# Performance work log

Measured on AMD Instinct MI355X. Metric: run time of the kernel, lower is better.

## Reference

```python
import jax, jax.numpy as jnp
import numpy as np


def setup_inputs() -> dict:
    key = jax.random.key(0)
    k1, k2, k3, k4, k5 = jax.random.split(key, 5)
    b, t_q, t_k = 4, 256, 1024
    qs, ms, n = 512, 512, 128
    return {
        "query": jax.random.normal(k1, (b, t_q, qs), dtype=jnp.float32),
        "keys": jax.random.normal(k2, (b, t_k, ms), dtype=jnp.float32),
        "Wq": jax.random.normal(k3, (qs, n), dtype=jnp.float32) * 0.05,
        "Wk": jax.random.normal(k4, (ms, n), dtype=jnp.float32) * 0.05,
        "linear_att": jax.random.normal(k5, (n,), dtype=jnp.float32) * 0.05,
    }


def reference(query, keys, Wq, Wk, linear_att):
    # projections: b t_q n and b t_k n
    att_query = jnp.einsum("bqd,dn->bqn", query, Wq)
    att_keys = jnp.einsum("bkd,dn->bkn", keys, Wk)
    # Bahdanau additive score: tanh(q + k) . v  -> b t_q t_k
    sum_qk = att_query[:, :, None, :] + att_keys[:, None, :, :]
    scores = jnp.einsum("bqkn,n->bqk", jnp.tanh(sum_qk), linear_att)
    weights = jax.nn.softmax(scores, axis=-1)
    context = jnp.einsum("bqk,bkd->bqd", weights, keys)
    return (context, weights)
```

## Files before the change

kernel.cpp:

```cpp
#include <hip/hip_runtime.h>

#define B 4
#define TQ 256
#define TK 1024
#define QS 512
#define NN 128

#define TANH_SCALE 2.8853900817779268f
#define LOG2E 1.4426950408889634f

__device__ __forceinline__ float fast_exp2(float x) {
#if __has_builtin(__builtin_amdgcn_exp2f)
    return __builtin_amdgcn_exp2f(x);
#else
    return exp2f(x);
#endif
}
__device__ __forceinline__ float fast_rcp(float x) {
#if __has_builtin(__builtin_amdgcn_rcpf)
    return __builtin_amdgcn_rcpf(x);
#else
    return 1.0f / x;
#endif
}

__global__ __launch_bounds__(256) void proj_kernel(
    const float* __restrict__ query, const float* __restrict__ keys,
    const float* __restrict__ Wq, const float* __restrict__ Wk,
    float* __restrict__ attq, float* __restrict__ attkT)
{
    __shared__ float As[32][18];
    __shared__ float Bs[32][132];

    const int tid = threadIdx.x;
    const int rb = blockIdx.x * 16;
    const bool isq = (rb < B * TQ);
    const float* A = isq ? (query + (size_t)rb * QS)
                         : (keys + (size_t)(rb - B * TQ) * QS);
    const float* W = isq ? Wq : Wk;

    const int n0 = (tid & 31) * 4;
    const int q0 = (tid >> 5) * 2;
    float acc[2][4] = {};

    for (int k0 = 0; k0 < QS; k0 += 32) {
        {
            const int r = tid >> 4, c = tid & 15;
            const float2 v = *(const float2*)(A + (size_t)r * QS + k0 + c * 2);
            As[c * 2 + 0][r] = v.x;
            As[c * 2 + 1][r] = v.y;
        }
        {
            const int n = (tid & 31) * 4, r0 = tid >> 5;
            #pragma unroll
            for (int j = 0; j < 4; ++j) {
                const int kk = r0 + j * 8;
                *(float4*)&Bs[kk][n] =
                    *(const float4*)(W + (size_t)(k0 + kk) * NN + n);
            }
        }
        __syncthreads();
        #pragma unroll
        for (int kk = 0; kk < 32; ++kk) {
            const float2 a = *(const float2*)&As[kk][q0];
            const float4 b = *(const float4*)&Bs[kk][n0];
            acc[0][0] = fmaf(a.x, b.x, acc[0][0]);
            acc[0][1] = fmaf(a.x, b.y, acc[0][1]);
            acc[0][2] = fmaf(a.x, b.z, acc[0][2]);
            acc[0][3] = fmaf(a.x, b.w, acc[0][3]);
            acc[1][0] = fmaf(a.y, b.x, acc[1][0]);
            acc[1][1] = fmaf(a.y, b.y, acc[1][1]);
            acc[1][2] = fmaf(a.y, b.z, acc[1][2]);
            acc[1][3] = fmaf(a.y, b.w, acc[1][3]);
        }
        __syncthreads();
    }

    if (isq) {
        float* out = attq + (size_t)rb * NN;
        #pragma unroll
        for (int i = 0; i < 2; ++i) {
            float4 o;
            o.x = acc[i][0] * TANH_SCALE;
            o.y = acc[i][1] * TANH_SCALE;
            o.z = acc[i][2] * TANH_SCALE;
            o.w = acc[i][3] * TANH_SCALE;
            *(float4*)(out + (size_t)(q0 + i) * NN + n0) = o;
        }
    } else {
        #pragma unroll
        for (int i = 0; i < 2; ++i) {
            float4 o;
            o.x = acc[i][0] * TANH_SCALE;
            o.y = acc[i][1] * TANH_SCALE;
            o.z = acc[i][2] * TANH_SCALE;
            o.w = acc[i][3] * TANH_SCALE;
            *(float4*)&Bs[q0 + i][n0] = o;
        }
        __syncthreads();
        const int rk = rb - B * TQ;
        const int bb = rk >> 10;
        const int kbase = rk & 1023;
        const int n = tid >> 1;
        const int kh = (tid & 1) * 8;
        float* o = attkT + (size_t)bb * NN * TK + (size_t)n * TK + kbase + kh;
        #pragma unroll
        for (int m4 = 0; m4 < 2; ++m4) {
            float4 t;
            t.x = Bs[kh + m4 * 4 + 0][n];
            t.y = Bs[kh + m4 * 4 + 1][n];
            t.z = Bs[kh + m4 * 4 + 2][n];
            t.w = Bs[kh + m4 * 4 + 3][n];
            *(float4*)(o + m4 * 4) = t;
        }
    }
}

__global__ __launch_bounds__(256) void score_softmax_kernel(
    const float* __restrict__ attq, const float* __restrict__ attkT,
    const float* __restrict__ vatt, float* __restrict__ wout)
{
    __shared__ float aqs[2][128];
    __shared__ float vsm[128];
    __shared__ float red[2][8];

    const int tid = threadIdx.x;
    const int b = blockIdx.x >> 7;
    const int q0 = (blockIdx.x & 127) * 2;

    if (tid < 128) {
        aqs[0][tid] = attq[((size_t)b * TQ + q0) * NN + tid];
        vsm[tid] = vatt[tid];
    } else {
        aqs[1][tid & 127] = attq[((size_t)b * TQ + q0 + 1) * NN + (tid & 127)];
    }
    __syncthreads();

    const float* kt = attkT + (size_t)b * NN * TK + (size_t)tid * 4;
    float s[2][4] = {};

    #pragma unroll 8
    for (int n = 0; n < 128; ++n) {
        const float4 a = *(const float4*)(kt + (size_t)n * TK);
        const float a0 = aqs[0][n], a1 = aqs[1][n], vv = vsm[n];
        const float av[4] = {a.x, a.y, a.z, a.w};
        #pragma unroll
        for (int r = 0; r < 4; ++r) {
            const float x0 = a0 + av[r];
            const float t0 = fmaf(-2.f, fast_rcp(1.f + fast_exp2(x0)), 1.f);
            s[0][r] = fmaf(vv, t0, s[0][r]);
            const float x1 = a1 + av[r];
            const float t1 = fmaf(-2.f, fast_rcp(1.f + fast_exp2(x1)), 1.f);
            s[1][r] = fmaf(vv, t1, s[1][r]);
        }
    }

    const int lane = tid & 63, wid = tid >> 6;
    #pragma unroll
    for (int qq = 0; qq < 2; ++qq) {
        float mm = fmaxf(fmaxf(s[qq][0], s[qq][1]), fmaxf(s[qq][2], s[qq][3]));
        #pragma unroll
        for (int off = 32; off > 0; off >>= 1)
            mm = fmaxf(mm, __shfl_xor(mm, off, 64));
        if (lane == 0) red[qq][wid] = mm;
    }
    __syncthreads();
    float m[2];
    m[0] = fmaxf(fmaxf(red[0][0], red[0][1]), fmaxf(red[0][2], red[0][3]));
    m[1] = fmaxf(fmaxf(red[1][0], red[1][1]), fmaxf(red[1][2], red[1][3]));

    float e[2][4];
    #pragma unroll
    for (int qq = 0; qq < 2; ++qq) {
        float ls = 0.f;
        #pragma unroll
        for (int i = 0; i < 4; ++i) {
            e[qq][i] = fast_exp2((s[qq][i] - m[qq]) * LOG2E);
            ls += e[qq][i];
        }
        #pragma unroll
        for (int off = 32; off > 0; off >>= 1)
            ls += __shfl_xor(ls, off, 64);
        if (lane == 0) red[qq][4 + wid] = ls;
    }
    __syncthreads();
    #pragma unroll
    for (int qq = 0; qq < 2; ++qq) {
        const float S = red[qq][4] + red[qq][5] + red[qq][6] + red[qq][7];
        const float inv = fast_rcp(S);
        float4 w4;
        w4.x = e[qq][0] * inv; w4.y = e[qq][1] * inv;
        w4.z = e[qq][2] * inv; w4.w = e[qq][3] * inv;
        *(float4*)(wout + ((size_t)b * TQ + q0 + qq) * TK + (size_t)tid * 4) = w4;
    }
}

#define CTX_ELEMS ((size_t)B * TQ * QS)

__global__ __launch_bounds__(256) void context_kernel(
    const float* __restrict__ keys, const float* __restrict__ w,
    float* __restrict__ ctxp)
{
    __shared__ float Wst[32][34];
    __shared__ float Ks[32][64];

    const int tid = threadIdx.x;
    const int bid = blockIdx.x;
    const int b = bid >> 8;
    const int rem = bid & 255;
    const int qt = rem >> 5;
    const int dt = (rem >> 2) & 7;
    const int ks = rem & 3;

    const float* wb = w + (size_t)b * TQ * TK + (size_t)qt * 32 * TK + ks * 256;
    const float* kb = keys + (size_t)b * TK * QS + (size_t)ks * 256 * QS + dt * 64;

    const int d0 = (tid & 15) * 4;
    const int q0 = (tid >> 4) * 2;
    float acc[2][4] = {};

    for (int k0 = 0; k0 < 256; k0 += 32) {
        {
            const int r = tid >> 3, c = tid & 7;
            const float4 v = *(const float4*)(wb + (size_t)r * TK + k0 + c * 4);
            Wst[c * 4 + 0][r] = v.x;
            Wst[c * 4 + 1][r] = v.y;
            Wst[c * 4 + 2][r] = v.z;
            Wst[c * 4 + 3][r] = v.w;
        }
        {
            const int c = tid & 15, r = tid >> 4;
            *(float4*)&Ks[r][c * 4] =
                *(const float4*)(kb + (size_t)(k0 + r) * QS + c * 4);
            *(float4*)&Ks[r + 16][c * 4] =
                *(const float4*)(kb + (size_t)(k0 + r + 16) * QS + c * 4);
        }
        __syncthreads();
        #pragma unroll
        for (int kk = 0; kk < 32; ++kk) {
            const float2 a = *(const float2*)&Wst[kk][q0];
            const float4 bb = *(const float4*)&Ks[kk][d0];
            acc[0][0] = fmaf(a.x, bb.x, acc[0][0]);
            acc[0][1] = fmaf(a.x, bb.y, acc[0][1]);
            acc[0][2] = fmaf(a.x, bb.z, acc[0][2]);
            acc[0][3] = fmaf(a.x, bb.w, acc[0][3]);
            acc[1][0] = fmaf(a.y, bb.x, acc[1][0]);
            acc[1][1] = fmaf(a.y, bb.y, acc[1][1]);
            acc[1][2] = fmaf(a.y, bb.z, acc[1][2]);
            acc[1][3] = fmaf(a.y, bb.w, acc[1][3]);
        }
        __syncthreads();
    }

    float* op = ctxp + (size_t)ks * CTX_ELEMS
              + ((size_t)b * TQ + qt * 32 + q0) * QS + dt * 64 + d0;
    #pragma unroll
    for (int i = 0; i < 2; ++i) {
        float4 o;
        o.x = acc[i][0]; o.y = acc[i][1]; o.z = acc[i][2]; o.w = acc[i][3];
        *(float4*)(op + (size_t)i * QS) = o;
    }
}

__global__ __launch_bounds__(256) void reduce_kernel(
    const float4* __restrict__ ctxp, float4* __restrict__ ctx)
{
    const size_t idx = (size_t)blockIdx.x * 256 + threadIdx.x;
    const size_t stride = CTX_ELEMS / 4;
    const float4 a = ctxp[idx];
    const float4 b = ctxp[idx + stride];
    const float4 c = ctxp[idx + 2 * stride];
    const float4 d = ctxp[idx + 3 * stride];
    float4 o;
    o.x = (a.x + b.x) + (c.x + d.x);
    o.y = (a.y + b.y) + (c.y + d.y);
    o.z = (a.z + b.z) + (c.z + d.z);
    o.w = (a.w + b.w) + (c.w + d.w);
    ctx[idx] = o;
}

extern "C" void kernel_launch(void* const* d_in, const int* in_sizes, int n_in,
                              void* d_out, int out_size, void* d_ws, size_t ws_size,
                              hipStream_t stream) {
    const float* query = (const float*)d_in[0];
    const float* keys  = (const float*)d_in[1];
    const float* Wq    = (const float*)d_in[2];
    const float* Wk    = (const float*)d_in[3];
    const float* vatt  = (const float*)d_in[4];

    float* ctx = (float*)d_out;
    float* wts = ctx + CTX_ELEMS;

    float* attq  = (float*)d_ws;
    float* attkT = attq + (size_t)B * TQ * NN;
    float* ctxp  = attkT + (size_t)B * NN * TK;

    hipLaunchKernelGGL(proj_kernel, dim3((B * TQ + B * TK) / 16), dim3(256), 0,
                       stream, query, keys, Wq, Wk, attq, attkT);
    hipLaunchKernelGGL(score_softmax_kernel, dim3(B * TQ / 2), dim3(256), 0,
                       stream, attq, attkT, vatt, wts);
    hipLaunchKernelGGL(context_kernel, dim3(1024), dim3(256), 0,
                       stream, keys, wts, ctxp);
    hipLaunchKernelGGL(reduce_kernel, dim3((unsigned)(CTX_ELEMS / 4 / 256)), dim3(256), 0,
                       stream, (const float4*)ctxp, (float4*)ctx);
}
```

Baseline: 149.5 us.

## Fuse four stage kernels into one cooperative kernel with grid syncs

Replaces the four separate launches (projection, score+softmax, context GEMM, split-K reduce) with a single cooperative kernel of 512 blocks that separates the stages with grid.sync and unions their shared memory. The context stage now splits K two ways instead of four, so the reduce reads only two partials. This removes launch gaps between kernels, but it caps parallelism at 512 resident blocks and adds grid-wide barrier cost. Stages that previously used more blocks (the 1024-block context GEMM) now run with fewer, longer blocks.

```diff
diff --git a/kernel.cpp b/kernel.cpp
--- a/kernel.cpp
+++ b/kernel.cpp
@@ -1,4 +1,7 @@
 #include <hip/hip_runtime.h>
+#include <hip/hip_cooperative_groups.h>
+
+namespace cg = cooperative_groups;
 
 #define B 4
 #define TQ 256
@@ -8,6 +11,7 @@
 
 #define TANH_SCALE 2.8853900817779268f
 #define LOG2E 1.4426950408889634f
+#define CTX_ELEMS ((size_t)B * TQ * QS)
 
 __device__ __forceinline__ float fast_exp2(float x) {
 #if __has_builtin(__builtin_amdgcn_exp2f)
@@ -24,259 +28,261 @@
 #endif
 }
 
-__global__ __launch_bounds__(256) void proj_kernel(
+union SmemU {
+    struct { float As[32][18]; float Bs[32][132]; } p1;
+    struct { float aqs[2][128]; float vsm[128]; float red[2][8]; } p2;
+    struct { float Wst[32][34]; float Ks[32][64]; } p3;
+};
+
+__global__ __launch_bounds__(256, 2) void fused_kernel(
     const float* __restrict__ query, const float* __restrict__ keys,
     const float* __restrict__ Wq, const float* __restrict__ Wk,
-    float* __restrict__ attq, float* __restrict__ attkT)
+    const float* __restrict__ vatt,
+    float* __restrict__ attq, float* __restrict__ attkT,
+    float* __restrict__ ctxp, float* __restrict__ ctx,
+    float* __restrict__ wout)
 {
-    __shared__ float As[32][18];
-    __shared__ float Bs[32][132];
-
+    __shared__ SmemU sm;
+    cg::grid_group grid = cg::this_grid();
     const int tid = threadIdx.x;
-    const int rb = blockIdx.x * 16;
-    const bool isq = (rb < B * TQ);
-    const float* A = isq ? (query + (size_t)rb * QS)
-                         : (keys + (size_t)(rb - B * TQ) * QS);
-    const float* W = isq ? Wq : Wk;
-
-    const int n0 = (tid & 31) * 4;
-    const int q0 = (tid >> 5) * 2;
-    float acc[2][4] = {};
-
-    for (int k0 = 0; k0 < QS; k0 += 32) {
-        {
-            const int r = tid >> 4, c = tid & 15;
-            const float2 v = *(const float2*)(A + (size_t)r * QS + k0 + c * 2);
-            As[c * 2 + 0][r] = v.x;
-            As[c * 2 + 1][r] = v.y;
-        }
-        {
-            const int n = (tid & 31) * 4, r0 = tid >> 5;
-            #pragma unroll
-            for (int j = 0; j < 4; ++j) {
-                const int kk = r0 + j * 8;
-                *(float4*)&Bs[kk][n] =
-                    *(const float4*)(W + (size_t)(k0 + kk) * NN + n);
-            }
+    const int bid = blockIdx.x;
+
+    if (bid < 320) {
+        const int rb = bid * 16;
+        const bool isq = (rb < B * TQ);
+        const float* A = isq ? (query + (size_t)rb * QS)
+                             : (keys + (size_t)(rb - B * TQ) * QS);
+        const float* W = isq ? Wq : Wk;
+
+        const int n0 = (tid & 31) * 4;
+        const int q0 = (tid >> 5) * 2;
+        float acc[2][4] = {};
+
+        for (int k0 = 0; k0 < QS; k0 += 32) {
+            {
+                const int r = tid >> 4, c = tid & 15;
+                const float2 v = *(const float2*)(A + (size_t)r * QS + k0 + c * 2);
+                sm.p1.As[c * 2 + 0][r] = v.x;
+                sm.p1.As[c * 2 + 1][r] = v.y;
+            }
+            {
+                const int n = (tid & 31) * 4, r0 = tid >> 5;
+                #pragma unroll
+                for (int j = 0; j < 4; ++j) {
+                    const int kk = r0 + j * 8;
+                    *(float4*)&sm.p1.Bs[kk][n] =
+                        *(const float4*)(W + (size_t)(k0 + kk) * NN + n);
+                }
+            }
+            __syncthreads();
+            #pragma unroll
+            for (int kk = 0; kk < 32; ++kk) {
+                const float2 a = *(const float2*)&sm.p1.As[kk][q0];
+                const float4 b = *(const float4*)&sm.p1.Bs[kk][n0];
+                acc[0][0] = fmaf(a.x, b.x, acc[0][0]);
+                acc[0][1] = fmaf(a.x, b.y, acc[0][1]);
+                acc[0][2] = fmaf(a.x, b.z, acc[0][2]);
+                acc[0][3] = fmaf(a.x, b.w, acc[0][3]);
+                acc[1][0] = fmaf(a.y, b.x, acc[1][0]);
+                acc[1][1] = fmaf(a.y, b.y, acc[1][1]);
+                acc[1][2] = fmaf(a.y, b.z, acc[1][2]);
+                acc[1][3] = fmaf(a.y, b.w, acc[1][3]);
+            }
+            __syncthreads();
+        }
+
+        if (isq) {
+            float* out = attq + (size_t)rb * NN;
+            #pragma unroll
+            for (int i = 0; i < 2; ++i) {
+                float4 o;
+                o.x = acc[i][0] * TANH_SCALE;
+                o.y = acc[i][1] * TANH_SCALE;
+                o.z = acc[i][2] * TANH_SCALE;
+                o.w = acc[i][3] * TANH_SCALE;
+                *(float4*)(out + (size_t)(q0 + i) * NN + n0) = o;
+            }
+        } else {
+            #pragma unroll
+            for (int i = 0; i < 2; ++i) {
+                float4 o;
+                o.x = acc[i][0] * TANH_SCALE;
+                o.y = acc[i][1] * TANH_SCALE;
+                o.z = acc[i][2] * TANH_SCALE;
+                o.w = acc[i][3] * TANH_SCALE;
+                *(float4*)&sm.p1.Bs[q0 + i][n0] = o;
+            }
+            __syncthreads();
+            const int rk = rb - B * TQ;
+            const int bb = rk >> 10;
+            const int kbase = rk & 1023;
+            const int n = tid >> 1;
+            const int kh = (tid & 1) * 8;
+            float* o = attkT + (size_t)bb * NN * TK + (size_t)n * TK + kbase + kh;
+            #pragma unroll
+            for (int m4 = 0; m4 < 2; ++m4) {
+                float4 t;
+                t.x = sm.p1.Bs[kh + m4 * 4 + 0][n];
+                t.y = sm.p1.Bs[kh + m4 * 4 + 1][n];
+                t.z = sm.p1.Bs[kh + m4 * 4 + 2][n];
+                t.w = sm.p1.Bs[kh + m4 * 4 + 3][n];
+                *(float4*)(o + m4 * 4) = t;
+            }
+        }
+    }
+    __threadfence();
+    grid.sync();
+
+    {
+        const int b = bid >> 7;
+        const int q0 = (bid & 127) * 2;
+
+        if (tid < 128) {
+            sm.p2.aqs[0][tid] = attq[((size_t)b * TQ + q0) * NN + tid];
+            sm.p2.vsm[tid] = vatt[tid];
+        } else {
+            sm.p2.aqs[1][tid & 127] =
+                attq[((size_t)b * TQ + q0 + 1) * NN + (tid & 127)];
+        }
+        __syncthreads();
+
+        const float* kt = attkT + (size_t)b * NN * TK + (size_t)tid * 4;
+        float s[2][4] = {};
+
+        #pragma unroll 8
+        for (int n = 0; n < 128; ++n) {
+            const float4 a = *(const float4*)(kt + (size_t)n * TK);
+            const float a0 = sm.p2.aqs[0][n], a1 = sm.p2.aqs[1][n];
+            const float vv = sm.p2.vsm[n];
+            const float av[4] = {a.x, a.y, a.z, a.w};
+            #pragma unroll
+            for (int r = 0; r < 4; ++r) {
+                const float x0 = a0 + av[r];
+                const float t0 = fmaf(-2.f, fast_rcp(1.f + fast_exp2(x0)), 1.f);
+                s[0][r] = fmaf(vv, t0, s[0][r]);
+                const float x1 = a1 + av[r];
+                const float t1 = fmaf(-2.f, fast_rcp(1.f + fast_exp2(x1)), 1.f);
+                s[1][r] = fmaf(vv, t1, s[1][r]);
+            }
+        }
+
+        const int lane = tid & 63, wid = tid >> 6;
+        #pragma unroll
+        for (int qq = 0; qq < 2; ++qq) {
+            float mm = fmaxf(fmaxf(s[qq][0], s[qq][1]), fmaxf(s[qq][2], s[qq][3]));
+            #pragma unroll
+            for (int off = 32; off > 0; off >>= 1)
+                mm = fmaxf(mm, __shfl_xor(mm, off, 64));
+            if (lane == 0) sm.p2.red[qq][wid] = mm;
+        }
+        __syncthreads();
+        float m[2];
+        m[0] = fmaxf(fmaxf(sm.p2.red[0][0], sm.p2.red[0][1]),
+                     fmaxf(sm.p2.red[0][2], sm.p2.red[0][3]));
+        m[1] = fmaxf(fmaxf(sm.p2.red[1][0], sm.p2.red[1][1]),
+                     fmaxf(sm.p2.red[1][2], sm.p2.red[1][3]));
+
+        float e[2][4];
+        #pragma unroll
+        for (int qq = 0; qq < 2; ++qq) {
+            float ls = 0.f;
+            #pragma unroll
+            for (int i = 0; i < 4; ++i) {
+                e[qq][i] = fast_exp2((s[qq][i] - m[qq]) * LOG2E);
+                ls += e[qq][i];
+            }
+            #pragma unroll
+            for (int off = 32; off > 0; off >>= 1)
+                ls += __shfl_xor(ls, off, 64);
+            if (lane == 0) sm.p2.red[qq][4 + wid] = ls;
         }
         __syncthreads();
         #pragma unroll
-        for (int kk = 0; kk < 32; ++kk) {
-            const float2 a = *(const float2*)&As[kk][q0];
-            const float4 b = *(const float4*)&Bs[kk][n0];
-            acc[0][0] = fmaf(a.x, b.x, acc[0][0]);
-            acc[0][1] = fmaf(a.x, b.y, acc[0][1]);
-            acc[0][2] = fmaf(a.x, b.z, acc[0][2]);
-            acc[0][3] = fmaf(a.x, b.w, acc[0][3]);
-            acc[1][0] = fmaf(a.y, b.x, acc[1][0]);
-            acc[1][1] = fmaf(a.y, b.y, acc[1][1]);
-            acc[1][2] = fmaf(a.y, b.z, acc[1][2]);
-            acc[1][3] = fmaf(a.y, b.w, acc[1][3]);
-        }
-        __syncthreads();
+        for (int qq = 0; qq < 2; ++qq) {
+            const float S = sm.p2.red[qq][4] + sm.p2.red[qq][5] +
+                            sm.p2.red[qq][6] + sm.p2.red[qq][7];
+            const float inv = fast_rcp(S);
+            float4 w4;
+            w4.x = e[qq][0] * inv; w4.y = e[qq][1] * inv;
+            w4.z = e[qq][2] * inv; w4.w = e[qq][3] * inv;
+            *(float4*)(wout + ((size_t)b * TQ + q0 + qq) * TK + (size_t)tid * 4) = w4;
+        }
     }
-
-    if (isq) {
-        float* out = attq + (size_t)rb * NN;
+    __threadfence();
+    grid.sync();
+
+    {
+        const int b = bid >> 7;
+        const int rem = bid & 127;
+        const int qt = rem >> 4;
+        const int dt = (rem >> 1) & 7;
+        const int ks = rem & 1;
+
+        const float* wb = wout + (size_t)b * TQ * TK + (size_t)qt * 32 * TK + ks * 512;
+        const float* kb = keys + (size_t)b * TK * QS + (size_t)ks * 512 * QS + dt * 64;
+
+        const int d0 = (tid & 15) * 4;
+        const int q0 = (tid >> 4) * 2;
+        float acc[2][4] = {};
+
+        for (int k0 = 0; k0 < 512; k0 += 32) {
+            {
+                const int r = tid >> 3, c = tid & 7;
+                const float4 v = *(const float4*)(wb + (size_t)r * TK + k0 + c * 4);
+                sm.p3.Wst[c * 4 + 0][r] = v.x;
+                sm.p3.Wst[c * 4 + 1][r] = v.y;
+                sm.p3.Wst[c * 4 + 2][r] = v.z;
+                sm.p3.Wst[c * 4 + 3][r] = v.w;
+            }
+            {
+                const int c = tid & 15, r = tid >> 4;
+                *(float4*)&sm.p3.Ks[r][c * 4] =
+                    *(const float4*)(kb + (size_t)(k0 + r) * QS + c * 4);
+                *(float4*)&sm.p3.Ks[r + 16][c * 4] =
+                    *(const float4*)(kb + (size_t)(k0 + r + 16) * QS + c * 4);
+            }
+            __syncthreads();
+            #pragma unroll
+            for (int kk = 0; kk < 32; ++kk) {
+                const float2 a = *(const float2*)&sm.p3.Wst[kk][q0];
+                const float4 bb = *(const float4*)&sm.p3.Ks[kk][d0];
+                acc[0][0] = fmaf(a.x, bb.x, acc[0][0]);
+                acc[0][1] = fmaf(a.x, bb.y, acc[0][1]);
+                acc[0][2] = fmaf(a.x, bb.z, acc[0][2]);
+                acc[0][3] = fmaf(a.x, bb.w, acc[0][3]);
+                acc[1][0] = fmaf(a.y, bb.x, acc[1][0]);
+                acc[1][1] = fmaf(a.y, bb.y, acc[1][1]);
+                acc[1][2] = fmaf(a.y, bb.z, acc[1][2]);
+                acc[1][3] = fmaf(a.y, bb.w, acc[1][3]);
+            }
+            __syncthreads();
+        }
+
+        float* op = ctxp + (size_t)ks * CTX_ELEMS
+                  + ((size_t)b * TQ + qt * 32 + q0) * QS + dt * 64 + d0;
         #pragma unroll
         for (int i = 0; i < 2; ++i) {
             float4 o;
-            o.x = acc[i][0] * TANH_SCALE;
-            o.y = acc[i][1] * TANH_SCALE;
-            o.z = acc[i][2] * TANH_SCALE;
-            o.w = acc[i][3] * TANH_SCALE;
-            *(float4*)(out + (size_t)(q0 + i) * NN + n0) = o;
-        }
-    } else {
-        #pragma unroll
-        for (int i = 0; i < 2; ++i) {
-            float4 o;
-            o.x = acc[i][0] * TANH_SCALE;
-            o.y = acc[i][1] * TANH_SCALE;
-            o.z = acc[i][2] * TANH_SCALE;
-            o.w = acc[i][3] * TANH_SCALE;
-            *(float4*)&Bs[q0 + i][n0] = o;
-        }
-        __syncthreads();
-        const int rk = rb - B * TQ;
-        const int bb = rk >> 10;
-        const int kbase = rk & 1023;
-        const int n = tid >> 1;
-        const int kh = (tid & 1) * 8;
-        float* o = attkT + (size_t)bb * NN * TK + (size_t)n * TK + kbase + kh;
-        #pragma unroll
-        for (int m4 = 0; m4 < 2; ++m4) {
-            float4 t;
-            t.x = Bs[kh + m4 * 4 + 0][n];
-            t.y = Bs[kh + m4 * 4 + 1][n];
-            t.z = Bs[kh + m4 * 4 + 2][n];
-            t.w = Bs[kh + m4 * 4 + 3][n];
-            *(float4*)(o + m4 * 4) = t;
+            o.x = acc[i][0]; o.y = acc[i][1]; o.z = acc[i][2]; o.w = acc[i][3];
+            *(float4*)(op + (size_t)i * QS) = o;
         }
     }
-}
-
-__global__ __launch_bounds__(256) void score_softmax_kernel(
-    const float* __restrict__ attq, const float* __restrict__ attkT,
-    const float* __restrict__ vatt, float* __restrict__ wout)
-{
-    __shared__ float aqs[2][128];
-    __shared__ float vsm[128];
-    __shared__ float red[2][8];
-
-    const int tid = threadIdx.x;
-    const int b = blockIdx.x >> 7;
-    const int q0 = (blockIdx.x & 127) * 2;
-
-    if (tid < 128) {
-        aqs[0][tid] = attq[((size_t)b * TQ + q0) * NN + tid];
-        vsm[tid] = vatt[tid];
-    } else {
-        aqs[1][tid & 127] = attq[((size_t)b * TQ + q0 + 1) * NN + (tid & 127)];
+    __threadfence();
+    grid.sync();
+
+    {
+        const size_t idx = (size_t)bid * 256 + tid;
+        const size_t stride = CTX_ELEMS / 4;
+        const float4* p = (const float4*)ctxp;
+        const float4 a = p[idx];
+        const float4 b4 = p[idx + stride];
+        float4 o;
+        o.x = a.x + b4.x;
+        o.y = a.y + b4.y;
+        o.z = a.z + b4.z;
+        o.w = a.w + b4.w;
+        ((float4*)ctx)[idx] = o;
     }
-    __syncthreads();
-
-    const float* kt = attkT + (size_t)b * NN * TK + (size_t)tid * 4;
-    float s[2][4] = {};
-
-    #pragma unroll 8
-    for (int n = 0; n < 128; ++n) {
-        const float4 a = *(const float4*)(kt + (size_t)n * TK);
-        const float a0 = aqs[0][n], a1 = aqs[1][n], vv = vsm[n];
-        const float av[4] = {a.x, a.y, a.z, a.w};
-        #pragma unroll
-        for (int r = 0; r < 4; ++r) {
-            const float x0 = a0 + av[r];
-            const float t0 = fmaf(-2.f, fast_rcp(1.f + fast_exp2(x0)), 1.f);
-            s[0][r] = fmaf(vv, t0, s[0][r]);
-            const float x1 = a1 + av[r];
-            const float t1 = fmaf(-2.f, fast_rcp(1.f + fast_exp2(x1)), 1.f);
-            s[1][r] = fmaf(vv, t1, s[1][r]);
-        }
-    }
-
-    const int lane = tid & 63, wid = tid >> 6;
-    #pragma unroll
-    for (int qq = 0; qq < 2; ++qq) {
-        float mm = fmaxf(fmaxf(s[qq][0], s[qq][1]), fmaxf(s[qq][2], s[qq][3]));
-        #pragma unroll
-        for (int off = 32; off > 0; off >>= 1)
-            mm = fmaxf(mm, __shfl_xor(mm, off, 64));
-        if (lane == 0) red[qq][wid] = mm;
-    }
-    __syncthreads();
-    float m[2];
-    m[0] = fmaxf(fmaxf(red[0][0], red[0][1]), fmaxf(red[0][2], red[0][3]));
-    m[1] = fmaxf(fmaxf(red[1][0], red[1][1]), fmaxf(red[1][2], red[1][3]));
-
-    float e[2][4];
-    #pragma unroll
-    for (int qq = 0; qq < 2; ++qq) {
-        float ls = 0.f;
-        #pragma unroll
-        for (int i = 0; i < 4; ++i) {
-            e[qq][i] = fast_exp2((s[qq][i] - m[qq]) * LOG2E);
-            ls += e[qq][i];
-        }
-        #pragma unroll
-        for (int off = 32; off > 0; off >>= 1)
-            ls += __shfl_xor(ls, off, 64);
-        if (lane == 0) red[qq][4 + wid] = ls;
-    }
-    __syncthreads();
-    #pragma unroll
-    for (int qq = 0; qq < 2; ++qq) {
-        const float S = red[qq][4] + red[qq][5] + red[qq][6] + red[qq][7];
-        const float inv = fast_rcp(S);
-        float4 w4;
-        w4.x = e[qq][0] * inv; w4.y = e[qq][1] * inv;
-        w4.z = e[qq][2] * inv; w4.w = e[qq][3] * inv;
-        *(float4*)(wout + ((size_t)b * TQ + q0 + qq) * TK + (size_t)tid * 4) = w4;
-    }
-}
-
-#define CTX_ELEMS ((size_t)B * TQ * QS)
-
-__global__ __launch_bounds__(256) void context_kernel(
-    const float* __restrict__ keys, const float* __restrict__ w,
-    float* __restrict__ ctxp)
-{
-    __shared__ float Wst[32][34];
-    __shared__ float Ks[32][64];
-
-    const int tid = threadIdx.x;
-    const int bid = blockIdx.x;
-    const int b = bid >> 8;
-    const int rem = bid & 255;
-    const int qt = rem >> 5;
-    const int dt = (rem >> 2) & 7;
-    const int ks = rem & 3;
-
-    const float* wb = w + (size_t)b * TQ * TK + (size_t)qt * 32 * TK + ks * 256;
-    const float* kb = keys + (size_t)b * TK * QS + (size_t)ks * 256 * QS + dt * 64;
-
-    const int d0 = (tid & 15) * 4;
-    const int q0 = (tid >> 4) * 2;
-    float acc[2][4] = {};
-
-    for (int k0 = 0; k0 < 256; k0 += 32) {
-        {
-            const int r = tid >> 3, c = tid & 7;
-            const float4 v = *(const float4*)(wb + (size_t)r * TK + k0 + c * 4);
-            Wst[c * 4 + 0][r] = v.x;
-            Wst[c * 4 + 1][r] = v.y;
-            Wst[c * 4 + 2][r] = v.z;
-            Wst[c * 4 + 3][r] = v.w;
-        }
-        {
-            const int c = tid & 15, r = tid >> 4;
-            *(float4*)&Ks[r][c * 4] =
-                *(const float4*)(kb + (size_t)(k0 + r) * QS + c * 4);
-            *(float4*)&Ks[r + 16][c * 4] =
-                *(const float4*)(kb + (size_t)(k0 + r + 16) * QS + c * 4);
-        }
-        __syncthreads();
-        #pragma unroll
-        for (int kk = 0; kk < 32; ++kk) {
-            const float2 a = *(const float2*)&Wst[kk][q0];
-            const float4 bb = *(const float4*)&Ks[kk][d0];
-            acc[0][0] = fmaf(a.x, bb.x, acc[0][0]);
-            acc[0][1] = fmaf(a.x, bb.y, acc[0][1]);
-            acc[0][2] = fmaf(a.x, bb.z, acc[0][2]);
-            acc[0][3] = fmaf(a.x, bb.w, acc[0][3]);
-            acc[1][0] = fmaf(a.y, bb.x, acc[1][0]);
-            acc[1][1] = fmaf(a.y, bb.y, acc[1][1]);
-            acc[1][2] = fmaf(a.y, bb.z, acc[1][2]);
-            acc[1][3] = fmaf(a.y, bb.w, acc[1][3]);
-        }
-        __syncthreads();
-    }
-
-    float* op = ctxp + (size_t)ks * CTX_ELEMS
-              + ((size_t)b * TQ + qt * 32 + q0) * QS + dt * 64 + d0;
-    #pragma unroll
-    for (int i = 0; i < 2; ++i) {
-        float4 o;
-        o.x = acc[i][0]; o.y = acc[i][1]; o.z = acc[i][2]; o.w = acc[i][3];
-        *(float4*)(op + (size_t)i * QS) = o;
-    }
-}
-
-__global__ __launch_bounds__(256) void reduce_kernel(
-    const float4* __restrict__ ctxp, float4* __restrict__ ctx)
-{
-    const size_t idx = (size_t)blockIdx.x * 256 + threadIdx.x;
-    const size_t stride = CTX_ELEMS / 4;
-    const float4 a = ctxp[idx];
-    const float4 b = ctxp[idx + stride];
-    const float4 c = ctxp[idx + 2 * stride];
-    const float4 d = ctxp[idx + 3 * stride];
-    float4 o;
-    o.x = (a.x + b.x) + (c.x + d.x);
-    o.y = (a.y + b.y) + (c.y + d.y);
-    o.z = (a.z + b.z) + (c.z + d.z);
-    o.w = (a.w + b.w) + (c.w + d.w);
-    ctx[idx] = o;
 }
 
 extern "C" void kernel_launch(void* const* d_in, const int* in_sizes, int n_in,
@@ -295,12 +301,10 @@
     float* attkT = attq + (size_t)B * TQ * NN;
     float* ctxp  = attkT + (size_t)B * NN * TK;
 
-    hipLaunchKernelGGL(proj_kernel, dim3((B * TQ + B * TK) / 16), dim3(256), 0,
-                       stream, query, keys, Wq, Wk, attq, attkT);
-    hipLaunchKernelGGL(score_softmax_kernel, dim3(B * TQ / 2), dim3(256), 0,
-                       stream, attq, attkT, vatt, wts);
-    hipLaunchKernelGGL(context_kernel, dim3(1024), dim3(256), 0,
-                       stream, keys, wts, ctxp);
-    hipLaunchKernelGGL(reduce_kernel, dim3((unsigned)(CTX_ELEMS / 4 / 256)), dim3(256), 0,
-                       stream, (const float4*)ctxp, (float4*)ctx);
+    void* args[] = {
+        (void*)&query, (void*)&keys, (void*)&Wq, (void*)&Wk, (void*)&vatt,
+        (void*)&attq, (void*)&attkT, (void*)&ctxp, (void*)&ctx, (void*)&wts,
+    };
+    hipLaunchCooperativeKernel((const void*)fused_kernel, dim3(512), dim3(256),
+                               args, 0, stream);
 }
```

Result: slower. 519.4 us (+247.5%).

## Fuse score, softmax and context matmul into one kernel per query group

Applied to the files above, without the earlier changes.

Merges the score/softmax kernel, the split-K context GEMM and the partial-sum reduction into one kernel. Each 512-thread block handles 4 queries, keeps their softmax weights in shared memory, and multiplies them against the keys directly, reducing the four k-split partials in shared memory. The block index is also remapped so that blocks of the same batch land on the same XCD. This removes two launches, the weights re-read and the partial-context round trip through global memory. In exchange, the context product now runs with only 256 blocks and 4 queries of reuse per key load, so keys are streamed far more times from L2, and large shared memory use may lower occupancy.

```diff
diff --git a/kernel.cpp b/kernel.cpp
--- a/kernel.cpp
+++ b/kernel.cpp
@@ -5,9 +5,11 @@
 #define TK 1024
 #define QS 512
 #define NN 128
+#define QPB 4
 
 #define TANH_SCALE 2.8853900817779268f
 #define LOG2E 1.4426950408889634f
+#define CTX_ELEMS ((size_t)B * TQ * QS)
 
 __device__ __forceinline__ float fast_exp2(float x) {
 #if __has_builtin(__builtin_amdgcn_exp2f)
@@ -116,167 +118,145 @@
     }
 }
 
-__global__ __launch_bounds__(256) void score_softmax_kernel(
+__global__ __launch_bounds__(512) void score_ctx_kernel(
     const float* __restrict__ attq, const float* __restrict__ attkT,
-    const float* __restrict__ vatt, float* __restrict__ wout)
+    const float* __restrict__ vatt, const float* __restrict__ keys,
+    float* __restrict__ wout, float* __restrict__ ctx)
 {
-    __shared__ float aqs[2][128];
-    __shared__ float vsm[128];
-    __shared__ float red[2][8];
+    __shared__ float aqs[QPB][NN];
+    __shared__ float vsm[NN];
+    __shared__ float red[QPB][8];
+    __shared__ float wls[QPB][TK];
+    __shared__ float rbuf[4][QPB][QS];
 
     const int tid = threadIdx.x;
-    const int b = blockIdx.x >> 7;
-    const int q0 = (blockIdx.x & 127) * 2;
-
-    if (tid < 128) {
-        aqs[0][tid] = attq[((size_t)b * TQ + q0) * NN + tid];
-        vsm[tid] = vatt[tid];
-    } else {
-        aqs[1][tid & 127] = attq[((size_t)b * TQ + q0 + 1) * NN + (tid & 127)];
-    }
-    __syncthreads();
-
-    const float* kt = attkT + (size_t)b * NN * TK + (size_t)tid * 4;
-    float s[2][4] = {};
-
-    #pragma unroll 8
-    for (int n = 0; n < 128; ++n) {
-        const float4 a = *(const float4*)(kt + (size_t)n * TK);
-        const float a0 = aqs[0][n], a1 = aqs[1][n], vv = vsm[n];
-        const float av[4] = {a.x, a.y, a.z, a.w};
-        #pragma unroll
-        for (int r = 0; r < 4; ++r) {
-            const float x0 = a0 + av[r];
+    const int bid = blockIdx.x;
+    const int xcd = bid & 7;
+    const int b = xcd >> 1;
+    const int qg = ((bid >> 3) << 1) | (xcd & 1);
+    const int q0 = qg * QPB;
+
+    if (tid < NN) vsm[tid] = vatt[tid];
+    if (tid < QPB * NN) {
+        const int qq = tid >> 7, nn = tid & 127;
+        aqs[qq][nn] = attq[((size_t)b * TQ + q0 + qq) * NN + nn];
+    }
+    __syncthreads();
+
+    const int k2 = tid * 2;
+    const float* kt = attkT + (size_t)b * NN * TK + k2;
+    float s[QPB][2] = {};
+
+    #pragma unroll 4
+    for (int n = 0; n < NN; ++n) {
+        const float2 a = *(const float2*)(kt + (size_t)n * TK);
+        const float vv = vsm[n];
+        #pragma unroll
+        for (int q = 0; q < QPB; ++q) {
+            const float aq = aqs[q][n];
+            const float x0 = aq + a.x;
             const float t0 = fmaf(-2.f, fast_rcp(1.f + fast_exp2(x0)), 1.f);
-            s[0][r] = fmaf(vv, t0, s[0][r]);
-            const float x1 = a1 + av[r];
+            s[q][0] = fmaf(vv, t0, s[q][0]);
+            const float x1 = aq + a.y;
             const float t1 = fmaf(-2.f, fast_rcp(1.f + fast_exp2(x1)), 1.f);
-            s[1][r] = fmaf(vv, t1, s[1][r]);
-        }
-    }
-
-    const int lane = tid & 63, wid = tid >> 6;
-    #pragma unroll
-    for (int qq = 0; qq < 2; ++qq) {
-        float mm = fmaxf(fmaxf(s[qq][0], s[qq][1]), fmaxf(s[qq][2], s[qq][3]));
+            s[q][1] = fmaf(vv, t1, s[q][1]);
+        }
+    }
+
+    const int lane = tid & 63, wv = tid >> 6;
+    #pragma unroll
+    for (int q = 0; q < QPB; ++q) {
+        float mm = fmaxf(s[q][0], s[q][1]);
         #pragma unroll
         for (int off = 32; off > 0; off >>= 1)
             mm = fmaxf(mm, __shfl_xor(mm, off, 64));
-        if (lane == 0) red[qq][wid] = mm;
-    }
-    __syncthreads();
-    float m[2];
-    m[0] = fmaxf(fmaxf(red[0][0], red[0][1]), fmaxf(red[0][2], red[0][3]));
-    m[1] = fmaxf(fmaxf(red[1][0], red[1][1]), fmaxf(red[1][2], red[1][3]));
-
-    float e[2][4];
-    #pragma unroll
-    for (int qq = 0; qq < 2; ++qq) {
-        float ls = 0.f;
-        #pragma unroll
-        for (int i = 0; i < 4; ++i) {
-            e[qq][i] = fast_exp2((s[qq][i] - m[qq]) * LOG2E);
-            ls += e[qq][i];
-        }
+        if (lane == 0) red[q][wv] = mm;
+    }
+    __syncthreads();
+    float m[QPB];
+    #pragma unroll
+    for (int q = 0; q < QPB; ++q) {
+        float mm = red[q][0];
+        #pragma unroll
+        for (int j = 1; j < 8; ++j) mm = fmaxf(mm, red[q][j]);
+        m[q] = mm;
+    }
+    __syncthreads();
+
+    float e[QPB][2];
+    #pragma unroll
+    for (int q = 0; q < QPB; ++q) {
+        e[q][0] = fast_exp2((s[q][0] - m[q]) * LOG2E);
+        e[q][1] = fast_exp2((s[q][1] - m[q]) * LOG2E);
+        float ls = e[q][0] + e[q][1];
         #pragma unroll
         for (int off = 32; off > 0; off >>= 1)
             ls += __shfl_xor(ls, off, 64);
-        if (lane == 0) red[qq][4 + wid] = ls;
-    }
-    __syncthreads();
-    #pragma unroll
-    for (int qq = 0; qq < 2; ++qq) {
-        const float S = red[qq][4] + red[qq][5] + red[qq][6] + red[qq][7];
+        if (lane == 0) red[q][wv] = ls;
+    }
+    __syncthreads();
+    #pragma unroll
+    for (int q = 0; q < QPB; ++q) {
+        float S = red[q][0];
+        #pragma unroll
+        for (int j = 1; j < 8; ++j) S += red[q][j];
         const float inv = fast_rcp(S);
-        float4 w4;
-        w4.x = e[qq][0] * inv; w4.y = e[qq][1] * inv;
-        w4.z = e[qq][2] * inv; w4.w = e[qq][3] * inv;
-        *(float4*)(wout + ((size_t)b * TQ + q0 + qq) * TK + (size_t)tid * 4) = w4;
-    }
-}
-
-#define CTX_ELEMS ((size_t)B * TQ * QS)
-
-__global__ __launch_bounds__(256) void context_kernel(
-    const float* __restrict__ keys, const float* __restrict__ w,
-    float* __restrict__ ctxp)
-{
-    __shared__ float Wst[32][34];
-    __shared__ float Ks[32][64];
-
-    const int tid = threadIdx.x;
-    const int bid = blockIdx.x;
-    const int b = bid >> 8;
-    const int rem = bid & 255;
-    const int qt = rem >> 5;
-    const int dt = (rem >> 2) & 7;
-    const int ks = rem & 3;
-
-    const float* wb = w + (size_t)b * TQ * TK + (size_t)qt * 32 * TK + ks * 256;
-    const float* kb = keys + (size_t)b * TK * QS + (size_t)ks * 256 * QS + dt * 64;
-
-    const int d0 = (tid & 15) * 4;
-    const int q0 = (tid >> 4) * 2;
-    float acc[2][4] = {};
-
-    for (int k0 = 0; k0 < 256; k0 += 32) {
-        {
-            const int r = tid >> 3, c = tid & 7;
-            const float4 v = *(const float4*)(wb + (size_t)r * TK + k0 + c * 4);
-            Wst[c * 4 + 0][r] = v.x;
-            Wst[c * 4 + 1][r] = v.y;
-            Wst[c * 4 + 2][r] = v.z;
-            Wst[c * 4 + 3][r] = v.w;
-        }
-        {
-            const int c = tid & 15, r = tid >> 4;
-            *(float4*)&Ks[r][c * 4] =
-                *(const float4*)(kb + (size_t)(k0 + r) * QS + c * 4);
-            *(float4*)&Ks[r + 16][c * 4] =
-                *(const float4*)(kb + (size_t)(k0 + r + 16) * QS + c * 4);
-        }
-        __syncthreads();
-        #pragma unroll
-        for (int kk = 0; kk < 32; ++kk) {
-            const float2 a = *(const float2*)&Wst[kk][q0];
-            const float4 bb = *(const float4*)&Ks[kk][d0];
-            acc[0][0] = fmaf(a.x, bb.x, acc[0][0]);
-            acc[0][1] = fmaf(a.x, bb.y, acc[0][1]);
-            acc[0][2] = fmaf(a.x, bb.z, acc[0][2]);
-            acc[0][3] = fmaf(a.x, bb.w, acc[0][3]);
-            acc[1][0] = fmaf(a.y, bb.x, acc[1][0]);
-            acc[1][1] = fmaf(a.y, bb.y, acc[1][1]);
-            acc[1][2] = fmaf(a.y, bb.z, acc[1][2]);
-            acc[1][3] = fmaf(a.y, bb.w, acc[1][3]);
-        }
-        __syncthreads();
-    }
-
-    float* op = ctxp + (size_t)ks * CTX_ELEMS
-              + ((size_t)b * TQ + qt * 32 + q0) * QS + dt * 64 + d0;
-    #pragma unroll
-    for (int i = 0; i < 2; ++i) {
-        float4 o;
-        o.x = acc[i][0]; o.y = acc[i][1]; o.z = acc[i][2]; o.w = acc[i][3];
-        *(float4*)(op + (size_t)i * QS) = o;
-    }
-}
-
-__global__ __launch_bounds__(256) void reduce_kernel(
-    const float4* __restrict__ ctxp, float4* __restrict__ ctx)
-{
-    const size_t idx = (size_t)blockIdx.x * 256 + threadIdx.x;
-    const size_t stride = CTX_ELEMS / 4;
-    const float4 a = ctxp[idx];
-    const float4 b = ctxp[idx + stride];
-    const float4 c = ctxp[idx + 2 * stride];
-    const float4 d = ctxp[idx + 3 * stride];
-    float4 o;
-    o.x = (a.x + b.x) + (c.x + d.x);
-    o.y = (a.y + b.y) + (c.y + d.y);
-    o.z = (a.z + b.z) + (c.z + d.z);
-    o.w = (a.w + b.w) + (c.w + d.w);
-    ctx[idx] = o;
+        float2 w2;
+        w2.x = e[q][0] * inv;
+        w2.y = e[q][1] * inv;
+        *(float2*)(wout + ((size_t)b * TQ + q0 + q) * TK + k2) = w2;
+        *(float2*)&wls[q][k2] = w2;
+    }
+    __syncthreads();
+
+    const int g = tid >> 7;
+    const int d0 = (tid & 127) * 4;
+    const float* kbp = keys + (size_t)b * TK * QS + d0;
+    float acc[QPB][4] = {};
+
+    const int kbeg = g * 256;
+    for (int k = kbeg; k < kbeg + 256; k += 4) {
+        float4 kv[4];
+        #pragma unroll
+        for (int i = 0; i < 4; ++i)
+            kv[i] = *(const float4*)(kbp + (size_t)(k + i) * QS);
+        #pragma unroll
+        for (int q = 0; q < QPB; ++q) {
+            const float4 wq = *(const float4*)&wls[q][k];
+            acc[q][0] = fmaf(wq.x, kv[0].x, acc[q][0]);
+            acc[q][1] = fmaf(wq.x, kv[0].y, acc[q][1]);
+            acc[q][2] = fmaf(wq.x, kv[0].z, acc[q][2]);
+            acc[q][3] = fmaf(wq.x, kv[0].w, acc[q][3]);
+            acc[q][0] = fmaf(wq.y, kv[1].x, acc[q][0]);
+            acc[q][1] = fmaf(wq.y, kv[1].y, acc[q][1]);
+            acc[q][2] = fmaf(wq.y, kv[1].z, acc[q][2]);
+            acc[q][3] = fmaf(wq.y, kv[1].w, acc[q][3]);
+            acc[q][0] = fmaf(wq.z, kv[2].x, acc[q][0]);
+            acc[q][1] = fmaf(wq.z, kv[2].y, acc[q][1]);
+            acc[q][2] = fmaf(wq.z, kv[2].z, acc[q][2]);
+            acc[q][3] = fmaf(wq.z, kv[2].w, acc[q][3]);
+            acc[q][0] = fmaf(wq.w, kv[3].x, acc[q][0]);
+            acc[q][1] = fmaf(wq.w, kv[3].y, acc[q][1]);
+            acc[q][2] = fmaf(wq.w, kv[3].z, acc[q][2]);
+            acc[q][3] = fmaf(wq.w, kv[3].w, acc[q][3]);
+        }
+    }
+
+    #pragma unroll
+    for (int q = 0; q < QPB; ++q)
+        *(float4*)&rbuf[g][q][d0] = *(float4*)&acc[q][0];
+    __syncthreads();
+
+    {
+        const int q = g;
+        float4 o = *(const float4*)&rbuf[0][q][d0];
+        #pragma unroll
+        for (int gg = 1; gg < 4; ++gg) {
+            const float4 p = *(const float4*)&rbuf[gg][q][d0];
+            o.x += p.x; o.y += p.y; o.z += p.z; o.w += p.w;
+        }
+        *(float4*)(ctx + ((size_t)b * TQ + q0 + q) * QS + d0) = o;
+    }
 }
 
 extern "C" void kernel_launch(void* const* d_in, const int* in_sizes, int n_in,
@@ -293,14 +273,9 @@
 
     float* attq  = (float*)d_ws;
     float* attkT = attq + (size_t)B * TQ * NN;
-    float* ctxp  = attkT + (size_t)B * NN * TK;
 
     hipLaunchKernelGGL(proj_kernel, dim3((B * TQ + B * TK) / 16), dim3(256), 0,
                        stream, query, keys, Wq, Wk, attq, attkT);
-    hipLaunchKernelGGL(score_softmax_kernel, dim3(B * TQ / 2), dim3(256), 0,
-                       stream, attq, attkT, vatt, wts);
-    hipLaunchKernelGGL(context_kernel, dim3(1024), dim3(256), 0,
-                       stream, keys, wts, ctxp);
-    hipLaunchKernelGGL(reduce_kernel, dim3((unsigned)(CTX_ELEMS / 4 / 256)), dim3(256), 0,
-                       stream, (const float4*)ctxp, (float4*)ctx);
-}
+    hipLaunchKernelGGL(score_ctx_kernel, dim3(B * TQ / QPB), dim3(512), 0,
+                       stream, attq, attkT, vatt, keys, wts, ctx);
+}
```

New measurement: 156.1 us. 1.04x slower.
